# Kernel tuning notes

Hardware: AMD Instinct MI355X
Metric: run time of the kernel (lower is better)

## Reference

```python
import jax, jax.numpy as jnp
import numpy as np
from jax import lax

N = 1024          # proposals per image
C = 32            # num classes (incl. background at index 0)
FEAT = 4096       # box-head feature dim
NDIM = 3          # voxel boxes, zyxzyx
SCORE_THRESH = 0.05
NMS_THR = 0.5
PER_CLS_TOPN = 300
DET_PER_IMG = 100
W_CTR = jnp.array([10.0, 10.0, 10.0])
W_SIZE = jnp.array([5.0, 5.0, 5.0])
BBOX_XFORM_CLIP = float(np.log(1000.0 / 16.0))
IMG_SIZE = jnp.array([96.0, 320.0, 320.0])


def decode_boxes(reg, boxes):
    # reg: [N, C, 6] (dz,dy,dx,dsz,dsy,dsx); boxes: [N, 6] zyxzyx, TO_REMOVE=1 convention
    sizes = boxes[:, 3:] - boxes[:, :3] + 1.0            # [N,3]
    ctrs = boxes[:, :3] + 0.5 * sizes                    # [N,3]
    d_ctr = reg[..., :3] / W_CTR                         # [N,C,3]
    d_size = jnp.minimum(reg[..., 3:] / W_SIZE, BBOX_XFORM_CLIP)
    pred_ctr = d_ctr * sizes[:, None, :] + ctrs[:, None, :]
    pred_size = jnp.exp(d_size) * sizes[:, None, :]
    mins = pred_ctr - 0.5 * pred_size
    maxs = pred_ctr + 0.5 * pred_size - 1.0
    return jnp.concatenate([mins, maxs], axis=-1)        # [N,C,6]


def iou3d(b):
    # b: [M,6] zyxzyx -> [M,M] IoU (volume with +1 convention)
    lt = jnp.maximum(b[:, None, :3], b[None, :, :3])
    rb = jnp.minimum(b[:, None, 3:], b[None, :, 3:])
    whd = jnp.clip(rb - lt + 1.0, 0.0)
    inter = whd.prod(-1)
    vol = jnp.clip(b[:, 3:] - b[:, :3] + 1.0, 0.0).prod(-1)
    return inter / (vol[:, None] + vol[None, :] - inter + 1e-12)


def per_class_nms(boxes_j, scores_j):
    # boxes_j: [N,6], scores_j: [N] (softmax probs for one foreground class)
    valid = scores_j > SCORE_THRESH
    s = jnp.where(valid, scores_j, -1.0)
    order = jnp.argsort(-s)                # sorted indices (score desc), padded at end
    sb = boxes_j[order]
    ss = s[order]
    sv = valid[order]
    M = iou3d(sb)
    idx = jnp.arange(N)

    def body(i, keep):
        sup = (M[i] > NMS_THR) & (idx > i) & keep[i] & sv[i]
        return keep & ~sup

    keep = lax.fori_loop(0, N, body, sv)
    keep = keep & sv
    rank = jnp.cumsum(keep.astype(jnp.int32)) - 1
    keep = keep & (rank < PER_CLS_TOPN)
    return sb, jnp.where(keep, ss, -1.0), order, keep


def _forward(features, class_logits, box_regression, proposal_boxes):
    probs = jax.nn.softmax(class_logits, axis=-1)        # [N,C]
    reg = box_regression.reshape(N, C, 2 * NDIM)
    boxes = decode_boxes(reg, proposal_boxes)            # [N,C,6]
    # clip_to_image (remove_empty=False)
    lim = IMG_SIZE - 1.0
    boxes = jnp.concatenate([jnp.clip(boxes[..., :3], 0.0, lim),
                             jnp.clip(boxes[..., 3:], 0.0, lim)], axis=-1)
    cls_boxes = jnp.swapaxes(boxes, 0, 1)[1:]            # [C-1,N,6] skip background
    cls_scores = probs.T[1:]                             # [C-1,N]
    sb, ss, order, keep = jax.vmap(per_class_nms)(cls_boxes, cls_scores)
    all_scores = ss.reshape(-1)                          # [(C-1)*N], -1 where dropped
    all_boxes = sb.reshape(-1, 2 * NDIM)
    all_orig = order.reshape(-1)
    all_labels = jnp.broadcast_to(jnp.arange(1, C)[:, None], (C - 1, N)).reshape(-1)
    # global sort by score desc, keep top detections_per_img
    top_s, top_i = lax.top_k(all_scores, DET_PER_IMG)
    valid = top_s > 0.0
    orig = all_orig[top_i]                               # original proposal index
    feats = jnp.where(valid[:, None], features[orig], 0.0)
    pboxes = jnp.where(valid[:, None], all_boxes[top_i], 0.0)
    pscores = jnp.where(valid, top_s, 0.0)
    plabels = jnp.where(valid, all_labels[top_i], 0)
    return feats, pboxes, pscores, plabels, valid


def setup_inputs() -> dict:
    key = jax.random.key(0)
    k1, k2, k3, k4, k5 = jax.random.split(key, 5)
    features = jax.random.normal(k1, (N, FEAT), dtype=jnp.float32)
    class_logits = 2.0 * jax.random.normal(k2, (N, C), dtype=jnp.float32)
    box_regression = jax.random.normal(k3, (N, C * 2 * NDIM), dtype=jnp.float32)
    img = np.array([96.0, 320.0, 320.0], dtype=np.float32)
    mins = jax.random.uniform(k4, (N, NDIM), dtype=jnp.float32) * (img * 0.75)
    ext = jax.random.uniform(k5, (N, NDIM), dtype=jnp.float32) * (img * 0.25) + 1.0
    proposal_boxes = jnp.concatenate([mins, mins + ext - 1.0], axis=-1)
    return {"features": features, "class_logits": class_logits,
            "box_regression": box_regression, "proposal_boxes": proposal_boxes}


def reference(features, class_logits, box_regression, proposal_boxes):
    return _forward(features, class_logits, box_regression, proposal_boxes)
```

## Files before the change

kernel.cpp:

```cpp
#include <hip/hip_runtime.h>
#include <math.h>

#define NPROP 1024
#define NCLS 32
#define FEATD 4096
#define SCORE_THRESH 0.05f
#define NMS_THR 0.5f
#define DET_PER_IMG 100
#define CLS_STRIDE 128
#define BBOX_CLIP 4.135166556742356f

__device__ __forceinline__ void wave_fence() {
    __builtin_amdgcn_wave_barrier();
    asm volatile("" ::: "memory");
}

__device__ __forceinline__ unsigned long long u64max(unsigned long long a,
                                                     unsigned long long b) {
    return a > b ? a : b;
}

__device__ __forceinline__ void decode_box(const float* __restrict__ prop,
                                           const float* __restrict__ reg,
                                           int n, int cls, float b[6]) {
    const float lim[3] = {95.0f, 319.0f, 319.0f};
    const float* r6 = reg + n * (NCLS * 6) + cls * 6;
#pragma unroll
    for (int d = 0; d < 3; ++d) {
        float lo = prop[n * 6 + d];
        float hi = prop[n * 6 + 3 + d];
        float sz = __fadd_rn(__fsub_rn(hi, lo), 1.0f);
        float ct = __fadd_rn(lo, __fmul_rn(0.5f, sz));
        float dc = r6[d] / 10.0f;
        float ds = fminf(r6[3 + d] / 5.0f, BBOX_CLIP);
        float pc = __fadd_rn(__fmul_rn(dc, sz), ct);
        float ps = __fmul_rn(expf(ds), sz);
        float hps = __fmul_rn(0.5f, ps);
        float mn = __fsub_rn(pc, hps);
        float mx = __fsub_rn(__fadd_rn(pc, hps), 1.0f);
        b[d]     = fminf(fmaxf(mn, 0.0f), lim[d]);
        b[3 + d] = fminf(fmaxf(mx, 0.0f), lim[d]);
    }
}

__global__ __launch_bounds__(1024) void nms_kernel(const float* __restrict__ logits,
                                                   const float* __restrict__ reg,
                                                   const float* __restrict__ prop,
                                                   float* __restrict__ scores_c,
                                                   int* __restrict__ orig_c,
                                                   int* __restrict__ counts) {
    const int cls = blockIdx.x + 1;
    const int tid = threadIdx.x;
    const int lane = tid & 63, wid = tid >> 6;

    __shared__ float s[NPROP];
    __shared__ int   order[NPROP];
    __shared__ float sb[NPROP][6];
    __shared__ float vols[NPROP];
    __shared__ unsigned long long keepw[16];
    __shared__ int   wtot[16];
    __shared__ int   kept_cum[2];

    const float* lrow = logits + tid * NCLS;
    float4 q[8];
#pragma unroll
    for (int r = 0; r < 8; ++r) q[r] = ((const float4*)lrow)[r];
    float m = -1e30f;
#pragma unroll
    for (int r = 0; r < 8; ++r)
        m = fmaxf(m, fmaxf(fmaxf(q[r].x, q[r].y), fmaxf(q[r].z, q[r].w)));
    float ssum = 0.0f;
#pragma unroll
    for (int r = 0; r < 8; ++r) {
        ssum += expf(q[r].x - m);
        ssum += expf(q[r].y - m);
        ssum += expf(q[r].z - m);
        ssum += expf(q[r].w - m);
    }
    float xc = lrow[cls];
    float p = expf(xc - m) / ssum;

    s[tid] = (p > SCORE_THRESH) ? p : -1.0f;
    order[tid] = tid;
    wave_fence();

    for (int k = 2; k <= NPROP; k <<= 1) {
        if (k >= 128) __syncthreads();
        for (int j = k >> 1; j > 0; j >>= 1) {
            int ixj = tid ^ j;
            if (ixj > tid) {
                float s0 = s[tid], s1 = s[ixj];
                int   i0 = order[tid], i1 = order[ixj];
                bool after = (s0 < s1) || (s0 == s1 && i0 > i1);
                bool dir = ((tid & k) == 0);
                if (after == dir) {
                    s[tid] = s1; s[ixj] = s0;
                    order[tid] = i1; order[ixj] = i0;
                }
            }
            if (j >= 64) __syncthreads();
            else wave_fence();
        }
    }
    __syncthreads();

    int o = order[tid];
    float myb[6];
    decode_box(prop, reg, o, cls, myb);
#pragma unroll
    for (int d = 0; d < 6; ++d) sb[tid][d] = myb[d];
    float myvol = 1.0f;
#pragma unroll
    for (int d = 0; d < 3; ++d)
        myvol *= fmaxf(myb[3 + d] - myb[d] + 1.0f, 0.0f);
    vols[tid] = myvol;

    float sv = s[tid];
    int mykeep = (sv > SCORE_THRESH) ? 1 : 0;
    unsigned long long m0 = __ballot(mykeep);
    if (lane == 0) keepw[wid] = m0;
    if (tid == 0) { kept_cum[0] = 0; kept_cum[1] = 0; }
    __syncthreads();

    for (int w = 0; w < 16; ++w) {
        if (kept_cum[w & 1] >= DET_PER_IMG) break;
        unsigned long long wk = 0;
        if (wid >= w) {
            wk = keepw[w];
            const int base = w << 6;
            if (wk) {
                float w0 = sb[base + lane][0], w1 = sb[base + lane][1];
                float w2 = sb[base + lane][2], w3 = sb[base + lane][3];
                float w4 = sb[base + lane][4], w5 = sb[base + lane][5];
                float wv = vols[base + lane];
                unsigned long long rest = wk;
                while (rest) {
                    int b = __ffsll((long long)rest) - 1;
                    rest &= rest - 1;
                    float b0 = sb[base + b][0], b1 = sb[base + b][1];
                    float b2 = sb[base + b][2], b3 = sb[base + b][3];
                    float b4 = sb[base + b][4], b5 = sb[base + b][5];
                    float bv = vols[base + b];
                    bool sup = false;
                    if (lane > b && ((wk >> lane) & 1)) {
                        float i0 = fmaxf(fminf(w3, b3) - fmaxf(w0, b0) + 1.0f, 0.0f);
                        float i1 = fmaxf(fminf(w4, b4) - fmaxf(w1, b1) + 1.0f, 0.0f);
                        float i2 = fmaxf(fminf(w5, b5) - fmaxf(w2, b2) + 1.0f, 0.0f);
                        float inter = i0 * i1 * i2;
                        sup = inter / (bv + wv - inter + 1e-12f) > NMS_THR;
                    }
                    unsigned long long supm = __ballot(sup);
                    wk &= ~supm;
                    rest &= ~supm;
                }
                if (wid == w) {
                    mykeep = (int)((wk >> lane) & 1);
                } else if (mykeep) {
                    unsigned long long t = wk;
                    while (t) {
                        int bb = __ffsll((long long)t) - 1;
                        t &= t - 1;
                        float b0 = sb[base + bb][0], b1 = sb[base + bb][1];
                        float b2 = sb[base + bb][2], b3 = sb[base + bb][3];
                        float b4 = sb[base + bb][4], b5 = sb[base + bb][5];
                        float bv = vols[base + bb];
                        float i0 = fmaxf(fminf(myb[3], b3) - fmaxf(myb[0], b0) + 1.0f, 0.0f);
                        float i1 = fmaxf(fminf(myb[4], b4) - fmaxf(myb[1], b1) + 1.0f, 0.0f);
                        float i2 = fmaxf(fminf(myb[5], b5) - fmaxf(myb[2], b2) + 1.0f, 0.0f);
                        float inter = i0 * i1 * i2;
                        if (inter / (bv + myvol - inter + 1e-12f) > NMS_THR) {
                            mykeep = 0;
                            break;
                        }
                    }
                }
            }
            if (wid == w && lane == 0)
                kept_cum[(w + 1) & 1] = kept_cum[w & 1] + __popcll(wk);
        }
        unsigned long long mm = __ballot(mykeep);
        if (lane == 0) keepw[wid] = mm;
        __syncthreads();
    }

    unsigned long long mask = __ballot(mykeep);
    int pre = __popcll(mask & ((1ull << lane) - 1ull));
    if (lane == 0) wtot[wid] = __popcll(mask);
    __syncthreads();
    int before = 0;
    for (int w = 0; w < wid; ++w) before += wtot[w];
    int rank = before + pre;

    if (mykeep && rank < DET_PER_IMG) {
        scores_c[(cls - 1) * CLS_STRIDE + rank] = sv;
        orig_c[(cls - 1) * CLS_STRIDE + rank] = order[tid];
    }
    if (tid == 0) {
        int tot = 0;
#pragma unroll
        for (int w = 0; w < 16; ++w) tot += wtot[w];
        counts[cls - 1] = tot < DET_PER_IMG ? tot : DET_PER_IMG;
    }
}

__global__ __launch_bounds__(64) void topk_kernel(const float* __restrict__ scores_c,
                                                  const int* __restrict__ counts,
                                                  float* __restrict__ tk_score,
                                                  int* __restrict__ tk_idx) {
    const int lane = threadIdx.x;
    int cnt = (lane < 31) ? counts[lane] : 0;
    if (cnt > DET_PER_IMG) cnt = DET_PER_IMG;

    unsigned long long head = 0;
    if (lane < 31 && cnt > 0) {
        unsigned u = __float_as_uint(scores_c[lane * CLS_STRIDE]) | 0x80000000u;
        head = ((unsigned long long)u << 32) | (unsigned)~(lane << 7);
    }

    for (int it = 0; it < DET_PER_IMG; ++it) {
        unsigned long long wb = head;
#pragma unroll
        for (int off = 1; off < 64; off <<= 1)
            wb = u64max(wb, (unsigned long long)__shfl_xor((long long)wb, off));
        if (wb == 0) {
            if (lane == 0) { tk_score[it] = -1.0f; tk_idx[it] = 0; }
            continue;
        }
        unsigned v = ~(unsigned)wb;
        if (lane == 0) {
            tk_score[it] = __uint_as_float((unsigned)(wb >> 32) & 0x7fffffffu);
            tk_idx[it] = (int)v;
        }
        int c = (int)(v >> 7), r = (int)(v & 127);
        if (lane == c) {
            int pos = r + 1;
            head = 0;
            if (pos < cnt) {
                unsigned u = __float_as_uint(scores_c[lane * CLS_STRIDE + pos]) | 0x80000000u;
                head = ((unsigned long long)u << 32) | (unsigned)~((lane << 7) | pos);
            }
        }
    }
}

__global__ void gather_kernel(const float* __restrict__ features,
                              const float* __restrict__ prop,
                              const float* __restrict__ reg,
                              const int* __restrict__ orig_c,
                              const float* __restrict__ tk_score,
                              const int* __restrict__ tk_idx,
                              float* __restrict__ out) {
    const int k = blockIdx.x;
    const int tid = threadIdx.x;
    float sc = tk_score[k];
    int flat = tk_idx[k];
    bool valid = sc > 0.0f;
    int cls = (flat >> 7) + 1;
    int orig = valid ? orig_c[flat] : 0;

    const float4* src = (const float4*)(features + (size_t)orig * FEATD);
    float4* dstf = (float4*)(out + (size_t)k * FEATD);
    const float4 z4 = make_float4(0.f, 0.f, 0.f, 0.f);
#pragma unroll
    for (int t = 0; t < 4; ++t) {
        int idx = tid + t * 256;
        dstf[idx] = valid ? src[idx] : z4;
    }

    const size_t boxOff = (size_t)DET_PER_IMG * FEATD;
    if (tid == 0) {
        float bb[6];
        decode_box(prop, reg, orig, cls, bb);
#pragma unroll
        for (int d = 0; d < 6; ++d)
            out[boxOff + k * 6 + d] = valid ? bb[d] : 0.0f;
    }
    if (tid == 1) out[boxOff + 600 + k] = valid ? sc : 0.0f;
    if (tid == 2) out[boxOff + 700 + k] = valid ? (float)cls : 0.0f;
    if (tid == 3) out[boxOff + 800 + k] = valid ? 1.0f : 0.0f;
}

extern "C" void kernel_launch(void* const* d_in, const int* in_sizes, int n_in,
                              void* d_out, int out_size, void* d_ws, size_t ws_size,
                              hipStream_t stream) {
    (void)in_sizes; (void)n_in; (void)out_size; (void)ws_size;
    const float* features = (const float*)d_in[0];
    const float* logits   = (const float*)d_in[1];
    const float* reg      = (const float*)d_in[2];
    const float* prop     = (const float*)d_in[3];
    float* out = (float*)d_out;

    float* scores_c = (float*)d_ws;
    int*   orig_c   = (int*)(scores_c + 31 * CLS_STRIDE);
    int*   counts   = (int*)(orig_c + 31 * CLS_STRIDE);
    float* tk_score = (float*)(counts + 32);
    int*   tk_idx   = (int*)(tk_score + DET_PER_IMG);

    nms_kernel<<<NCLS - 1, 1024, 0, stream>>>(logits, reg, prop,
                                              scores_c, orig_c, counts);
    topk_kernel<<<1, 64, 0, stream>>>(scores_c, counts, tk_score, tk_idx);
    gather_kernel<<<DET_PER_IMG, 256, 0, stream>>>(
        features, prop, reg, orig_c, tk_score, tk_idx, out);
}
```

Before: 176.4 us.

## Register-resident bitonic sort with packed keys and shuffles; stage top-k scores in LDS

The bitonic sort now keeps a packed 64-bit key per thread: a sign-flipped score in the high bits and the inverted index in the low bits. Strides below 64 are exchanged with wave shuffles, and larger strides go through a double-buffered shared array with one barrier per step. This replaces the shared-memory compare-and-swap over separate score and index arrays. Separately, the top-k kernel copies all per-class scores into LDS up front, so the serial merge loop no longer issues dependent global loads. The trade-off is a larger shared footprint, and the sort's correctness depends on the packed key ordering matching the original tie-break.

```diff
diff --git a/kernel.cpp b/kernel.cpp
--- a/kernel.cpp
+++ b/kernel.cpp
@@ -10,14 +10,23 @@
 #define CLS_STRIDE 128
 #define BBOX_CLIP 4.135166556742356f
 
-__device__ __forceinline__ void wave_fence() {
-    __builtin_amdgcn_wave_barrier();
-    asm volatile("" ::: "memory");
-}
-
 __device__ __forceinline__ unsigned long long u64max(unsigned long long a,
                                                      unsigned long long b) {
     return a > b ? a : b;
+}
+
+__device__ __forceinline__ unsigned flip_f32(float f) {
+    unsigned u = __float_as_uint(f);
+    return u ^ ((unsigned)(((int)u) >> 31) | 0x80000000u);
+}
+__device__ __forceinline__ float unflip_f32(unsigned u) {
+    u = (u & 0x80000000u) ? (u ^ 0x80000000u) : ~u;
+    return __uint_as_float(u);
+}
+
+__device__ __forceinline__ unsigned long long shfl_xor_u64(unsigned long long v,
+                                                           int mask) {
+    return (unsigned long long)__shfl_xor((long long)v, mask);
 }
 
 __device__ __forceinline__ void decode_box(const float* __restrict__ prop,
@@ -53,8 +62,7 @@
     const int tid = threadIdx.x;
     const int lane = tid & 63, wid = tid >> 6;
 
-    __shared__ float s[NPROP];
-    __shared__ int   order[NPROP];
+    __shared__ unsigned long long kbuf[2][NPROP];
     __shared__ float sb[NPROP][6];
     __shared__ float vols[NPROP];
     __shared__ unsigned long long keepw[16];
@@ -79,32 +87,32 @@
     }
     float xc = lrow[cls];
     float p = expf(xc - m) / ssum;
-
-    s[tid] = (p > SCORE_THRESH) ? p : -1.0f;
-    order[tid] = tid;
-    wave_fence();
-
+    float sv0 = (p > SCORE_THRESH) ? p : -1.0f;
+
+    unsigned long long key =
+        ((unsigned long long)flip_f32(sv0) << 32) | (unsigned)~tid;
+    int pb = 0;
     for (int k = 2; k <= NPROP; k <<= 1) {
-        if (k >= 128) __syncthreads();
         for (int j = k >> 1; j > 0; j >>= 1) {
-            int ixj = tid ^ j;
-            if (ixj > tid) {
-                float s0 = s[tid], s1 = s[ixj];
-                int   i0 = order[tid], i1 = order[ixj];
-                bool after = (s0 < s1) || (s0 == s1 && i0 > i1);
-                bool dir = ((tid & k) == 0);
-                if (after == dir) {
-                    s[tid] = s1; s[ixj] = s0;
-                    order[tid] = i1; order[ixj] = i0;
-                }
+            unsigned long long pk;
+            if (j >= 64) {
+                kbuf[pb][tid] = key;
+                __syncthreads();
+                pk = kbuf[pb][tid ^ j];
+                pb ^= 1;
+            } else {
+                pk = shfl_xor_u64(key, j);
             }
-            if (j >= 64) __syncthreads();
-            else wave_fence();
-        }
-    }
-    __syncthreads();
-
-    int o = order[tid];
+            bool lower = (tid & j) == 0;
+            bool desc  = (tid & k) == 0;
+            bool want_max = (lower == desc);
+            bool pk_gt = pk > key;
+            key = (want_max == pk_gt) ? pk : key;
+        }
+    }
+    float sv = unflip_f32((unsigned)(key >> 32));
+    int o = (int)(~(unsigned)key);
+
     float myb[6];
     decode_box(prop, reg, o, cls, myb);
 #pragma unroll
@@ -115,7 +123,6 @@
         myvol *= fmaxf(myb[3 + d] - myb[d] + 1.0f, 0.0f);
     vols[tid] = myvol;
 
-    float sv = s[tid];
     int mykeep = (sv > SCORE_THRESH) ? 1 : 0;
     unsigned long long m0 = __ballot(mykeep);
     if (lane == 0) keepw[wid] = m0;
@@ -193,7 +200,7 @@
 
     if (mykeep && rank < DET_PER_IMG) {
         scores_c[(cls - 1) * CLS_STRIDE + rank] = sv;
-        orig_c[(cls - 1) * CLS_STRIDE + rank] = order[tid];
+        orig_c[(cls - 1) * CLS_STRIDE + rank] = o;
     }
     if (tid == 0) {
         int tot = 0;
@@ -208,12 +215,22 @@
                                                   float* __restrict__ tk_score,
                                                   int* __restrict__ tk_idx) {
     const int lane = threadIdx.x;
+    __shared__ float lsc[31 * CLS_STRIDE];
+
+    const float4* src4 = (const float4*)scores_c;
+    float4* dst4 = (float4*)lsc;
+#pragma unroll
+    for (int t = 0; t < 16; ++t) {
+        int idx = t * 64 + lane;
+        if (idx < (31 * CLS_STRIDE) / 4) dst4[idx] = src4[idx];
+    }
     int cnt = (lane < 31) ? counts[lane] : 0;
     if (cnt > DET_PER_IMG) cnt = DET_PER_IMG;
+    __syncthreads();
 
     unsigned long long head = 0;
     if (lane < 31 && cnt > 0) {
-        unsigned u = __float_as_uint(scores_c[lane * CLS_STRIDE]) | 0x80000000u;
+        unsigned u = __float_as_uint(lsc[lane * CLS_STRIDE]) | 0x80000000u;
         head = ((unsigned long long)u << 32) | (unsigned)~(lane << 7);
     }
 
@@ -221,7 +238,7 @@
         unsigned long long wb = head;
 #pragma unroll
         for (int off = 1; off < 64; off <<= 1)
-            wb = u64max(wb, (unsigned long long)__shfl_xor((long long)wb, off));
+            wb = u64max(wb, shfl_xor_u64(wb, off));
         if (wb == 0) {
             if (lane == 0) { tk_score[it] = -1.0f; tk_idx[it] = 0; }
             continue;
@@ -236,7 +253,7 @@
             int pos = r + 1;
             head = 0;
             if (pos < cnt) {
-                unsigned u = __float_as_uint(scores_c[lane * CLS_STRIDE + pos]) | 0x80000000u;
+                unsigned u = __float_as_uint(lsc[lane * CLS_STRIDE + pos]) | 0x80000000u;
                 head = ((unsigned long long)u << 32) | (unsigned)~((lane << 7) | pos);
             }
         }
```

After: 172.7 us. 1.02x faster.
